# Kernel tuning notes

Hardware: AMD Instinct MI355X
Metric: run time of the kernel (lower is better)

## Reference

```python
import jax, jax.numpy as jnp
import numpy as np

N, M, D, E = 16384, 8192, 8, 2_000_000
DELTA = 1.0   # init arg delta
P = 1.0       # init arg p (forced to 1 in __init__)
EPS = 1e-6


def setup_inputs() -> dict:
    key = jax.random.key(0)
    ks = jax.random.split(key, 7)
    return {
        "gamma_rows": jax.random.normal(ks[0], (N,), dtype=jnp.float32),
        "gamma_cols": jax.random.normal(ks[1], (M,), dtype=jnp.float32),
        "latent_z": jax.random.uniform(ks[2], (N, D), dtype=jnp.float32),
        "latent_w": jax.random.uniform(ks[3], (M, D), dtype=jnp.float32),
        "weights": jax.random.uniform(ks[4], (E,), dtype=jnp.float32),
        "rows_idx": jax.random.randint(ks[5], (E,), 0, N, dtype=jnp.int32),
        "col_idx": jax.random.randint(ks[6], (E,), 0, M, dtype=jnp.int32),
    }


def reference(gamma_rows, gamma_cols, latent_z, latent_w, weights, rows_idx, col_idx):
    # Simplex projections (Softmax over latent dim)
    z = jax.nn.softmax(latent_z, axis=1)   # [N, D]
    w = jax.nn.softmax(latent_w, axis=1)   # [M, D]

    # torch.cdist(z, w, p=2): full N x M euclidean distance matrix
    sq = (jnp.sum(z * z, axis=1)[:, None]
          + jnp.sum(w * w, axis=1)[None, :]
          - 2.0 * (z @ w.T))                       # [N, M]
    dist = jnp.sqrt(jnp.maximum(sq, 0.0))          # [N, M]
    dist_matrix = -DELTA * (dist + EPS)            # [N, M]

    # z_pdist1 = exp(gamma_rows) @ exp(dist_matrix) @ exp(gamma_cols)
    z_pdist1 = jnp.einsum("i,ij,j->", jnp.exp(gamma_rows),
                          jnp.exp(dist_matrix), jnp.exp(gamma_cols))

    # Edge (link) term: per-edge euclidean distance between gathered embeddings
    delta_latent = jnp.sqrt(jnp.sum((z[rows_idx] - w[col_idx]) ** 2, axis=-1))  # [E]
    z_pdist2 = jnp.sum(weights * (gamma_rows[rows_idx] + gamma_cols[col_idx]
                                  - (DELTA * delta_latent) ** P))

    return -z_pdist2 + z_pdist1
```

## Files before the change

### kernel.cpp

```cpp
#include <hip/hip_runtime.h>
#include <math.h>

#define N_ROWS 16384
#define M_COLS 8192
#define TPB 256
#define IT 4
#define JT 64
#define JU 4
#define NJ (M_COLS / JT)
#define NIB (N_ROWS / (TPB * IT))
#define PAIR_BLOCKS (NIB * NJ)
#define EDGE_BLOCKS 2048
#define EU 4
#define GRID_BLOCKS (PAIR_BLOCKS + EDGE_BLOCKS)

typedef float v2f __attribute__((ext_vector_type(2)));
typedef _Float16 h8 __attribute__((ext_vector_type(8)));

#define C2 2.0813689810056077f

__global__ __launch_bounds__(TPB) void rownorm_kernel(
    const float* __restrict__ lz, const float* __restrict__ gr,
    const float* __restrict__ lw, const float* __restrict__ gc,
    float* __restrict__ z, float* __restrict__ zz, float* __restrict__ eg,
    _Float16* __restrict__ zh,
    float* __restrict__ w, float* __restrict__ ww, float* __restrict__ ec,
    _Float16* __restrict__ wh)
{
    int gi = blockIdx.x * TPB + threadIdx.x;
    const float *src, *g;
    float *dv, *dq, *de;
    _Float16* dh;
    int i;
    if (gi < N_ROWS) { src = lz; g = gr; dv = z; dq = zz; de = eg; dh = zh; i = gi; }
    else             { src = lw; g = gc; dv = w; dq = ww; de = ec; dh = wh; i = gi - N_ROWS; }

    const float4* sp = (const float4*)(src + (size_t)i * 8);
    float4 a = sp[0], b = sp[1];
    float v[8] = {a.x, a.y, a.z, a.w, b.x, b.y, b.z, b.w};
    float m = v[0];
    #pragma unroll
    for (int d = 1; d < 8; d++) m = fmaxf(m, v[d]);
    float s = 0.f;
    #pragma unroll
    for (int d = 0; d < 8; d++) { v[d] = __expf(v[d] - m); s += v[d]; }
    float inv = 1.f / s;
    float sq = 0.f;
    h8 hv;
    #pragma unroll
    for (int d = 0; d < 8; d++) {
        v[d] *= inv;
        sq = fmaf(v[d], v[d], sq);
        hv[d] = (_Float16)v[d];
    }
    float4 o0 = {v[0], v[1], v[2], v[3]};
    float4 o1 = {v[4], v[5], v[6], v[7]};
    float4* dp = (float4*)(dv + (size_t)i * 8);
    dp[0] = o0; dp[1] = o1;
    *(h8*)(dh + (size_t)i * 8) = hv;
    dq[i] = C2 * sq;
    de[i] = __expf(g[i]);
}

__global__ __launch_bounds__(TPB) void fused_kernel(
    const float* __restrict__ z, const float* __restrict__ zz,
    const float* __restrict__ eg,
    const float* __restrict__ w, const float* __restrict__ ww,
    const float* __restrict__ ec,
    const _Float16* __restrict__ zh, const _Float16* __restrict__ wh,
    const float* __restrict__ gr, const float* __restrict__ gc,
    const float* __restrict__ wt,
    const int* __restrict__ ridx, const int* __restrict__ cidx, int E,
    double* __restrict__ pair_part, double* __restrict__ edge_part)
{
    __shared__ float  sw[JT * 8];
    __shared__ float  swq[JT];
    __shared__ float  sec[JT];
    __shared__ double sred[TPB];

    const int t   = threadIdx.x;
    const int bid = blockIdx.x;
    const int rid = bid >> 1;

    if ((bid & 1) == 0) {
        const int ib = rid / NJ;
        const int jb = rid - ib * NJ;
        const int j0 = jb * JT;

        if (t < JT * 2) ((float4*)sw)[t] = ((const float4*)(w + (size_t)j0 * 8))[t];
        if (t < JT)     { swq[t] = ww[j0 + t]; sec[t] = ec[j0 + t]; }

        v2f  zi[IT][4];
        float zzi[IT], acc[IT];
        const int ibase = ib * (TPB * IT);
        #pragma unroll
        for (int k = 0; k < IT; k++) {
            int i = ibase + k * TPB + t;
            const float4* zp = (const float4*)(z + (size_t)i * 8);
            float4 a = zp[0], b = zp[1];
            zi[k][0] = (v2f){-2.f * C2 * a.x, -2.f * C2 * a.y};
            zi[k][1] = (v2f){-2.f * C2 * a.z, -2.f * C2 * a.w};
            zi[k][2] = (v2f){-2.f * C2 * b.x, -2.f * C2 * b.y};
            zi[k][3] = (v2f){-2.f * C2 * b.z, -2.f * C2 * b.w};
            zzi[k] = zz[i];
            acc[k] = 0.f;
        }
        __syncthreads();

        const float4* s4 = (const float4*)sw;
        for (int jo = 0; jo < JT; jo += JU) {
            float4 wa[JU], wb[JU];
            float  wq[JU], ev[JU];
            #pragma unroll
            for (int u = 0; u < JU; u++) {
                wa[u] = s4[(jo + u) * 2];
                wb[u] = s4[(jo + u) * 2 + 1];
                wq[u] = swq[jo + u];
                ev[u] = sec[jo + u];
            }
            float sq[JU][IT];
            #pragma unroll
            for (int u = 0; u < JU; u++) {
                v2f w01 = {wa[u].x, wa[u].y}, w23 = {wa[u].z, wa[u].w};
                v2f w45 = {wb[u].x, wb[u].y}, w67 = {wb[u].z, wb[u].w};
                #pragma unroll
                for (int k = 0; k < IT; k++) {
                    v2f p = {zzi[k], wq[u]};
                    p = __builtin_elementwise_fma(zi[k][0], w01, p);
                    p = __builtin_elementwise_fma(zi[k][1], w23, p);
                    p = __builtin_elementwise_fma(zi[k][2], w45, p);
                    p = __builtin_elementwise_fma(zi[k][3], w67, p);
                    sq[u][k] = fmaxf(p.x + p.y, 0.f);
                }
            }
            float dd[JU][IT];
            #pragma unroll
            for (int u = 0; u < JU; u++)
                #pragma unroll
                for (int k = 0; k < IT; k++)
                    asm("v_sqrt_f32 %0, %1" : "=v"(dd[u][k]) : "v"(sq[u][k]));
            float pr[JU][IT];
            #pragma unroll
            for (int u = 0; u < JU; u++)
                #pragma unroll
                for (int k = 0; k < IT; k++)
                    asm("v_exp_f32 %0, -%1" : "=v"(pr[u][k]) : "v"(dd[u][k]));
            #pragma unroll
            for (int u = 0; u < JU; u++)
                #pragma unroll
                for (int k = 0; k < IT; k++)
                    acc[k] = fmaf(ev[u], pr[u][k], acc[k]);
        }

        double tp = 0.0;
        #pragma unroll
        for (int k = 0; k < IT; k++) {
            int i = ibase + k * TPB + t;
            tp += (double)eg[i] * (double)acc[k];
        }

        sred[t] = tp;
        __syncthreads();
        for (int s = TPB / 2; s > 0; s >>= 1) {
            if (t < s) sred[t] += sred[t + s];
            __syncthreads();
        }
        if (t == 0) pair_part[rid] = sred[0];
    } else {
        const int tid = rid * TPB + t;
        const int e0 = tid * EU;
        double local = 0.0;
        if (e0 < E) {
            int4   rr  = *(const int4*)(ridx + e0);
            int4   cc  = *(const int4*)(cidx + e0);
            float4 wt4 = *(const float4*)(wt + e0);
            int   r[EU]  = {rr.x, rr.y, rr.z, rr.w};
            int   c[EU]  = {cc.x, cc.y, cc.z, cc.w};
            float wv[EU] = {wt4.x, wt4.y, wt4.z, wt4.w};
            h8 zr[EU], wr[EU];
            float grv[EU], gcv[EU];
            #pragma unroll
            for (int u = 0; u < EU; u++) {
                zr[u]  = *(const h8*)(zh + (size_t)r[u] * 8);
                wr[u]  = *(const h8*)(wh + (size_t)c[u] * 8);
                grv[u] = gr[r[u]];
                gcv[u] = gc[c[u]];
            }
            #pragma unroll
            for (int u = 0; u < EU; u++) {
                h8 dv = zr[u] - wr[u];
                float s = 0.f;
                #pragma unroll
                for (int qd = 0; qd < 8; qd++) {
                    float f = (float)dv[qd];
                    s = fmaf(f, f, s);
                }
                float dist;
                asm("v_sqrt_f32 %0, %1" : "=v"(dist) : "v"(s));
                local += (double)(wv[u] * (grv[u] + gcv[u] - dist));
            }
        }
        sred[t] = local;
        __syncthreads();
        for (int s2 = TPB / 2; s2 > 0; s2 >>= 1) {
            if (t < s2) sred[t] += sred[t + s2];
            __syncthreads();
        }
        if (t == 0) edge_part[rid] = sred[0];
    }
}

__global__ __launch_bounds__(TPB) void final_kernel(
    const double* __restrict__ pp, int np,
    const double* __restrict__ ep, int ne,
    float* __restrict__ out)
{
    __shared__ double sred[TPB];
    const int t = threadIdx.x;
    double s1 = 0.0, s2 = 0.0;
    for (int i = t; i < np; i += TPB) s1 += pp[i];
    for (int i = t; i < ne; i += TPB) s2 += ep[i];
    sred[t] = s1;
    __syncthreads();
    for (int s = TPB / 2; s > 0; s >>= 1) {
        if (t < s) sred[t] += sred[t + s];
        __syncthreads();
    }
    double pair_sum = sred[0];
    __syncthreads();
    sred[t] = s2;
    __syncthreads();
    for (int s = TPB / 2; s > 0; s >>= 1) {
        if (t < s) sred[t] += sred[t + s];
        __syncthreads();
    }
    if (t == 0) {
        double edge_sum = sred[0];
        double cf = exp(-1.0e-6);
        out[0] = (float)(cf * pair_sum - edge_sum);
    }
}

extern "C" void kernel_launch(void* const* d_in, const int* in_sizes, int n_in,
                              void* d_out, int out_size, void* d_ws, size_t ws_size,
                              hipStream_t stream)
{
    const float* gamma_rows = (const float*)d_in[0];
    const float* gamma_cols = (const float*)d_in[1];
    const float* latent_z   = (const float*)d_in[2];
    const float* latent_w   = (const float*)d_in[3];
    const float* weights    = (const float*)d_in[4];
    const int*   rows_idx   = (const int*)d_in[5];
    const int*   col_idx    = (const int*)d_in[6];
    float* out = (float*)d_out;
    const int E = in_sizes[4];

    char* base = (char*)d_ws;
    size_t off = 0;
    float* z  = (float*)(base + off); off += (size_t)N_ROWS * 8 * 4;
    float* zz = (float*)(base + off); off += (size_t)N_ROWS * 4;
    float* eg = (float*)(base + off); off += (size_t)N_ROWS * 4;
    float* w  = (float*)(base + off); off += (size_t)M_COLS * 8 * 4;
    float* ww = (float*)(base + off); off += (size_t)M_COLS * 4;
    float* ec = (float*)(base + off); off += (size_t)M_COLS * 4;
    _Float16* zh = (_Float16*)(base + off); off += (size_t)N_ROWS * 8 * 2;
    _Float16* wh = (_Float16*)(base + off); off += (size_t)M_COLS * 8 * 2;
    double* pair_part = (double*)(base + off); off += (size_t)PAIR_BLOCKS * 8;
    double* edge_part = (double*)(base + off); off += (size_t)EDGE_BLOCKS * 8;
    (void)ws_size;

    rownorm_kernel<<<(N_ROWS + M_COLS) / TPB, TPB, 0, stream>>>(
        latent_z, gamma_rows, latent_w, gamma_cols,
        z, zz, eg, zh, w, ww, ec, wh);
    fused_kernel<<<GRID_BLOCKS, TPB, 0, stream>>>(
        z, zz, eg, w, ww, ec, zh, wh, gamma_rows, gamma_cols,
        weights, rows_idx, col_idx, E, pair_part, edge_part);
    final_kernel<<<1, TPB, 0, stream>>>(pair_part, PAIR_BLOCKS,
                                        edge_part, EDGE_BLOCKS, out);
}
```

Baseline: 171.6 us.

## Split fused pair/edge kernel into separate launches with scalar FMAs and direct loads

Replaces the interleaved pair/edge single kernel with two separate kernels launched back to back. The pair kernel drops the shared-memory staging of w tiles and the barrier, reading w, ww and ec directly from global memory with uniform addresses (likely scalar loads). It also replaces packed v2f FMAs with scalar fmaf chains. This removes branch divergence between block types and the LDS sync, but gives up overlap between the compute-bound pair work and the memory-bound edge gathers, and may lose packed-FMA throughput.

```diff
diff --git a/kernel.cpp b/kernel.cpp
--- a/kernel.cpp
+++ b/kernel.cpp
@@ -12,9 +12,7 @@
 #define PAIR_BLOCKS (NIB * NJ)
 #define EDGE_BLOCKS 2048
 #define EU 4
-#define GRID_BLOCKS (PAIR_BLOCKS + EDGE_BLOCKS)
-
-typedef float v2f __attribute__((ext_vector_type(2)));
+
 typedef _Float16 h8 __attribute__((ext_vector_type(8)));
 
 #define C2 2.0813689810056077f
@@ -62,152 +60,142 @@
     de[i] = __expf(g[i]);
 }
 
-__global__ __launch_bounds__(TPB) void fused_kernel(
+__global__ __launch_bounds__(TPB) void pair_kernel(
     const float* __restrict__ z, const float* __restrict__ zz,
     const float* __restrict__ eg,
     const float* __restrict__ w, const float* __restrict__ ww,
     const float* __restrict__ ec,
+    double* __restrict__ pair_part)
+{
+    __shared__ double sred[TPB];
+    const int t   = threadIdx.x;
+    const int rid = blockIdx.x;
+    const int ib  = rid / NJ;
+    const int jb  = rid - ib * NJ;
+    const int j0  = jb * JT;
+
+    float zi[IT][8], zzi[IT], acc[IT];
+    const int ibase = ib * (TPB * IT);
+    #pragma unroll
+    for (int k = 0; k < IT; k++) {
+        int i = ibase + k * TPB + t;
+        const float4* zp = (const float4*)(z + (size_t)i * 8);
+        float4 a = zp[0], b = zp[1];
+        zi[k][0] = -2.f * C2 * a.x; zi[k][1] = -2.f * C2 * a.y;
+        zi[k][2] = -2.f * C2 * a.z; zi[k][3] = -2.f * C2 * a.w;
+        zi[k][4] = -2.f * C2 * b.x; zi[k][5] = -2.f * C2 * b.y;
+        zi[k][6] = -2.f * C2 * b.z; zi[k][7] = -2.f * C2 * b.w;
+        zzi[k] = zz[i];
+        acc[k] = 0.f;
+    }
+
+    const float* wb  = w  + (size_t)j0 * 8;
+    const float* wqb = ww + j0;
+    const float* ecb = ec + j0;
+
+    for (int jo = 0; jo < JT; jo += JU) {
+        float wv[JU][8], wq[JU], ev[JU];
+        #pragma unroll
+        for (int u = 0; u < JU; u++) {
+            #pragma unroll
+            for (int d = 0; d < 8; d++) wv[u][d] = wb[(jo + u) * 8 + d];
+            wq[u] = wqb[jo + u];
+            ev[u] = ecb[jo + u];
+        }
+        float sq[JU][IT];
+        #pragma unroll
+        for (int u = 0; u < JU; u++) {
+            #pragma unroll
+            for (int k = 0; k < IT; k++) {
+                float p = zzi[k] + wq[u];
+                #pragma unroll
+                for (int d = 0; d < 8; d++) p = fmaf(zi[k][d], wv[u][d], p);
+                sq[u][k] = fmaxf(p, 0.f);
+            }
+        }
+        float dd[JU][IT];
+        #pragma unroll
+        for (int u = 0; u < JU; u++)
+            #pragma unroll
+            for (int k = 0; k < IT; k++)
+                asm("v_sqrt_f32 %0, %1" : "=v"(dd[u][k]) : "v"(sq[u][k]));
+        float pr[JU][IT];
+        #pragma unroll
+        for (int u = 0; u < JU; u++)
+            #pragma unroll
+            for (int k = 0; k < IT; k++)
+                asm("v_exp_f32 %0, -%1" : "=v"(pr[u][k]) : "v"(dd[u][k]));
+        #pragma unroll
+        for (int u = 0; u < JU; u++)
+            #pragma unroll
+            for (int k = 0; k < IT; k++)
+                acc[k] = fmaf(ev[u], pr[u][k], acc[k]);
+    }
+
+    double tp = 0.0;
+    #pragma unroll
+    for (int k = 0; k < IT; k++) {
+        int i = ibase + k * TPB + t;
+        tp += (double)eg[i] * (double)acc[k];
+    }
+    sred[t] = tp;
+    __syncthreads();
+    for (int s = TPB / 2; s > 0; s >>= 1) {
+        if (t < s) sred[t] += sred[t + s];
+        __syncthreads();
+    }
+    if (t == 0) pair_part[rid] = sred[0];
+}
+
+__global__ __launch_bounds__(TPB) void edge_kernel(
     const _Float16* __restrict__ zh, const _Float16* __restrict__ wh,
     const float* __restrict__ gr, const float* __restrict__ gc,
     const float* __restrict__ wt,
     const int* __restrict__ ridx, const int* __restrict__ cidx, int E,
-    double* __restrict__ pair_part, double* __restrict__ edge_part)
-{
-    __shared__ float  sw[JT * 8];
-    __shared__ float  swq[JT];
-    __shared__ float  sec[JT];
+    double* __restrict__ edge_part)
+{
     __shared__ double sred[TPB];
-
     const int t   = threadIdx.x;
-    const int bid = blockIdx.x;
-    const int rid = bid >> 1;
-
-    if ((bid & 1) == 0) {
-        const int ib = rid / NJ;
-        const int jb = rid - ib * NJ;
-        const int j0 = jb * JT;
-
-        if (t < JT * 2) ((float4*)sw)[t] = ((const float4*)(w + (size_t)j0 * 8))[t];
-        if (t < JT)     { swq[t] = ww[j0 + t]; sec[t] = ec[j0 + t]; }
-
-        v2f  zi[IT][4];
-        float zzi[IT], acc[IT];
-        const int ibase = ib * (TPB * IT);
-        #pragma unroll
-        for (int k = 0; k < IT; k++) {
-            int i = ibase + k * TPB + t;
-            const float4* zp = (const float4*)(z + (size_t)i * 8);
-            float4 a = zp[0], b = zp[1];
-            zi[k][0] = (v2f){-2.f * C2 * a.x, -2.f * C2 * a.y};
-            zi[k][1] = (v2f){-2.f * C2 * a.z, -2.f * C2 * a.w};
-            zi[k][2] = (v2f){-2.f * C2 * b.x, -2.f * C2 * b.y};
-            zi[k][3] = (v2f){-2.f * C2 * b.z, -2.f * C2 * b.w};
-            zzi[k] = zz[i];
-            acc[k] = 0.f;
-        }
-        __syncthreads();
-
-        const float4* s4 = (const float4*)sw;
-        for (int jo = 0; jo < JT; jo += JU) {
-            float4 wa[JU], wb[JU];
-            float  wq[JU], ev[JU];
-            #pragma unroll
-            for (int u = 0; u < JU; u++) {
-                wa[u] = s4[(jo + u) * 2];
-                wb[u] = s4[(jo + u) * 2 + 1];
-                wq[u] = swq[jo + u];
-                ev[u] = sec[jo + u];
+    const int tid = blockIdx.x * TPB + t;
+    const int e0  = tid * EU;
+    double local = 0.0;
+    if (e0 < E) {
+        int4   rr  = *(const int4*)(ridx + e0);
+        int4   cc  = *(const int4*)(cidx + e0);
+        float4 wt4 = *(const float4*)(wt + e0);
+        int   r[EU]  = {rr.x, rr.y, rr.z, rr.w};
+        int   c[EU]  = {cc.x, cc.y, cc.z, cc.w};
+        float wv[EU] = {wt4.x, wt4.y, wt4.z, wt4.w};
+        h8 zr[EU], wr[EU];
+        float grv[EU], gcv[EU];
+        #pragma unroll
+        for (int u = 0; u < EU; u++) {
+            zr[u]  = *(const h8*)(zh + (size_t)r[u] * 8);
+            wr[u]  = *(const h8*)(wh + (size_t)c[u] * 8);
+            grv[u] = gr[r[u]];
+            gcv[u] = gc[c[u]];
+        }
+        #pragma unroll
+        for (int u = 0; u < EU; u++) {
+            h8 dv = zr[u] - wr[u];
+            float s = 0.f;
+            #pragma unroll
+            for (int qd = 0; qd < 8; qd++) {
+                float f = (float)dv[qd];
+                s = fmaf(f, f, s);
             }
-            float sq[JU][IT];
-            #pragma unroll
-            for (int u = 0; u < JU; u++) {
-                v2f w01 = {wa[u].x, wa[u].y}, w23 = {wa[u].z, wa[u].w};
-                v2f w45 = {wb[u].x, wb[u].y}, w67 = {wb[u].z, wb[u].w};
-                #pragma unroll
-                for (int k = 0; k < IT; k++) {
-                    v2f p = {zzi[k], wq[u]};
-                    p = __builtin_elementwise_fma(zi[k][0], w01, p);
-                    p = __builtin_elementwise_fma(zi[k][1], w23, p);
-                    p = __builtin_elementwise_fma(zi[k][2], w45, p);
-                    p = __builtin_elementwise_fma(zi[k][3], w67, p);
-                    sq[u][k] = fmaxf(p.x + p.y, 0.f);
-                }
-            }
-            float dd[JU][IT];
-            #pragma unroll
-            for (int u = 0; u < JU; u++)
-                #pragma unroll
-                for (int k = 0; k < IT; k++)
-                    asm("v_sqrt_f32 %0, %1" : "=v"(dd[u][k]) : "v"(sq[u][k]));
-            float pr[JU][IT];
-            #pragma unroll
-            for (int u = 0; u < JU; u++)
-                #pragma unroll
-                for (int k = 0; k < IT; k++)
-                    asm("v_exp_f32 %0, -%1" : "=v"(pr[u][k]) : "v"(dd[u][k]));
-            #pragma unroll
-            for (int u = 0; u < JU; u++)
-                #pragma unroll
-                for (int k = 0; k < IT; k++)
-                    acc[k] = fmaf(ev[u], pr[u][k], acc[k]);
-        }
-
-        double tp = 0.0;
-        #pragma unroll
-        for (int k = 0; k < IT; k++) {
-            int i = ibase + k * TPB + t;
-            tp += (double)eg[i] * (double)acc[k];
-        }
-
-        sred[t] = tp;
-        __syncthreads();
-        for (int s = TPB / 2; s > 0; s >>= 1) {
-            if (t < s) sred[t] += sred[t + s];
-            __syncthreads();
-        }
-        if (t == 0) pair_part[rid] = sred[0];
-    } else {
-        const int tid = rid * TPB + t;
-        const int e0 = tid * EU;
-        double local = 0.0;
-        if (e0 < E) {
-            int4   rr  = *(const int4*)(ridx + e0);
-            int4   cc  = *(const int4*)(cidx + e0);
-            float4 wt4 = *(const float4*)(wt + e0);
-            int   r[EU]  = {rr.x, rr.y, rr.z, rr.w};
-            int   c[EU]  = {cc.x, cc.y, cc.z, cc.w};
-            float wv[EU] = {wt4.x, wt4.y, wt4.z, wt4.w};
-            h8 zr[EU], wr[EU];
-            float grv[EU], gcv[EU];
-            #pragma unroll
-            for (int u = 0; u < EU; u++) {
-                zr[u]  = *(const h8*)(zh + (size_t)r[u] * 8);
-                wr[u]  = *(const h8*)(wh + (size_t)c[u] * 8);
-                grv[u] = gr[r[u]];
-                gcv[u] = gc[c[u]];
-            }
-            #pragma unroll
-            for (int u = 0; u < EU; u++) {
-                h8 dv = zr[u] - wr[u];
-                float s = 0.f;
-                #pragma unroll
-                for (int qd = 0; qd < 8; qd++) {
-                    float f = (float)dv[qd];
-                    s = fmaf(f, f, s);
-                }
-                float dist;
-                asm("v_sqrt_f32 %0, %1" : "=v"(dist) : "v"(s));
-                local += (double)(wv[u] * (grv[u] + gcv[u] - dist));
-            }
-        }
-        sred[t] = local;
-        __syncthreads();
-        for (int s2 = TPB / 2; s2 > 0; s2 >>= 1) {
-            if (t < s2) sred[t] += sred[t + s2];
-            __syncthreads();
-        }
-        if (t == 0) edge_part[rid] = sred[0];
-    }
+            float dist;
+            asm("v_sqrt_f32 %0, %1" : "=v"(dist) : "v"(s));
+            local += (double)(wv[u] * (grv[u] + gcv[u] - dist));
+        }
+    }
+    sred[t] = local;
+    __syncthreads();
+    for (int s2 = TPB / 2; s2 > 0; s2 >>= 1) {
+        if (t < s2) sred[t] += sred[t + s2];
+        __syncthreads();
+    }
+    if (t == 0) edge_part[blockIdx.x] = sred[0];
 }
 
 __global__ __launch_bounds__(TPB) void final_kernel(
@@ -272,9 +260,10 @@
     rownorm_kernel<<<(N_ROWS + M_COLS) / TPB, TPB, 0, stream>>>(
         latent_z, gamma_rows, latent_w, gamma_cols,
         z, zz, eg, zh, w, ww, ec, wh);
-    fused_kernel<<<GRID_BLOCKS, TPB, 0, stream>>>(
-        z, zz, eg, w, ww, ec, zh, wh, gamma_rows, gamma_cols,
-        weights, rows_idx, col_idx, E, pair_part, edge_part);
+    pair_kernel<<<PAIR_BLOCKS, TPB, 0, stream>>>(
+        z, zz, eg, w, ww, ec, pair_part);
+    edge_kernel<<<EDGE_BLOCKS, TPB, 0, stream>>>(
+        zh, wh, gamma_rows, gamma_cols, weights, rows_idx, col_idx, E, edge_part);
     final_kernel<<<1, TPB, 0, stream>>>(pair_part, PAIR_BLOCKS,
                                         edge_part, EDGE_BLOCKS, out);
 }
```

Result: no change. 173.4 us (+1.1%).

## Pack fp16 embedding with gamma per row, double edge unroll, rebalance block interleave

Applied to the files above, without the earlier changes.

Each row's fp16 softmax vector and its gamma value now sit together in one 32-byte record, so each edge gathers one cache line per endpoint instead of two separate random loads. The edge path handles 8 edges per thread across 1024 blocks, and blocks are interleaved two pair blocks to one edge block. The pair inner loop also moves the norm-sum add out of the FMA chain. This cuts scattered gather traffic and gives each thread more loads in flight, at the cost of more registers in edge blocks and a slightly longer dependent add in the pair loop.

```diff
diff --git a/kernel.cpp b/kernel.cpp
--- a/kernel.cpp
+++ b/kernel.cpp
@@ -10,30 +10,31 @@
 #define NJ (M_COLS / JT)
 #define NIB (N_ROWS / (TPB * IT))
 #define PAIR_BLOCKS (NIB * NJ)
-#define EDGE_BLOCKS 2048
-#define EU 4
+#define EDGE_BLOCKS 1024
+#define EU 8
 #define GRID_BLOCKS (PAIR_BLOCKS + EDGE_BLOCKS)
 
 typedef float v2f __attribute__((ext_vector_type(2)));
 typedef _Float16 h8 __attribute__((ext_vector_type(8)));
 
 #define C2 2.0813689810056077f
+#define ROWB 32
 
 __global__ __launch_bounds__(TPB) void rownorm_kernel(
     const float* __restrict__ lz, const float* __restrict__ gr,
     const float* __restrict__ lw, const float* __restrict__ gc,
     float* __restrict__ z, float* __restrict__ zz, float* __restrict__ eg,
-    _Float16* __restrict__ zh,
+    char* __restrict__ zpack,
     float* __restrict__ w, float* __restrict__ ww, float* __restrict__ ec,
-    _Float16* __restrict__ wh)
+    char* __restrict__ wpack)
 {
     int gi = blockIdx.x * TPB + threadIdx.x;
     const float *src, *g;
     float *dv, *dq, *de;
-    _Float16* dh;
+    char* dp8;
     int i;
-    if (gi < N_ROWS) { src = lz; g = gr; dv = z; dq = zz; de = eg; dh = zh; i = gi; }
-    else             { src = lw; g = gc; dv = w; dq = ww; de = ec; dh = wh; i = gi - N_ROWS; }
+    if (gi < N_ROWS) { src = lz; g = gr; dv = z; dq = zz; de = eg; dp8 = zpack; i = gi; }
+    else             { src = lw; g = gc; dv = w; dq = ww; de = ec; dp8 = wpack; i = gi - N_ROWS; }
 
     const float4* sp = (const float4*)(src + (size_t)i * 8);
     float4 a = sp[0], b = sp[1];
@@ -53,13 +54,16 @@
         sq = fmaf(v[d], v[d], sq);
         hv[d] = (_Float16)v[d];
     }
+    float gam = g[i];
     float4 o0 = {v[0], v[1], v[2], v[3]};
     float4 o1 = {v[4], v[5], v[6], v[7]};
     float4* dp = (float4*)(dv + (size_t)i * 8);
     dp[0] = o0; dp[1] = o1;
-    *(h8*)(dh + (size_t)i * 8) = hv;
     dq[i] = C2 * sq;
-    de[i] = __expf(g[i]);
+    de[i] = __expf(gam);
+    char* rp = dp8 + (size_t)i * ROWB;
+    *(h8*)rp = hv;
+    *(float*)(rp + 16) = gam;
 }
 
 __global__ __launch_bounds__(TPB) void fused_kernel(
@@ -67,8 +71,7 @@
     const float* __restrict__ eg,
     const float* __restrict__ w, const float* __restrict__ ww,
     const float* __restrict__ ec,
-    const _Float16* __restrict__ zh, const _Float16* __restrict__ wh,
-    const float* __restrict__ gr, const float* __restrict__ gc,
+    const char* __restrict__ zpack, const char* __restrict__ wpack,
     const float* __restrict__ wt,
     const int* __restrict__ ridx, const int* __restrict__ cidx, int E,
     double* __restrict__ pair_part, double* __restrict__ edge_part)
@@ -80,9 +83,11 @@
 
     const int t   = threadIdx.x;
     const int bid = blockIdx.x;
-    const int rid = bid >> 1;
-
-    if ((bid & 1) == 0) {
+    const int tri = bid / 3;
+    const int rem = bid - tri * 3;
+
+    if (rem != 0) {
+        const int rid = tri * 2 + (rem - 1);
         const int ib = rid / NJ;
         const int jb = rid - ib * NJ;
         const int j0 = jb * JT;
@@ -125,12 +130,11 @@
                 v2f w45 = {wb[u].x, wb[u].y}, w67 = {wb[u].z, wb[u].w};
                 #pragma unroll
                 for (int k = 0; k < IT; k++) {
-                    v2f p = {zzi[k], wq[u]};
-                    p = __builtin_elementwise_fma(zi[k][0], w01, p);
+                    v2f p = zi[k][0] * w01;
                     p = __builtin_elementwise_fma(zi[k][1], w23, p);
                     p = __builtin_elementwise_fma(zi[k][2], w45, p);
                     p = __builtin_elementwise_fma(zi[k][3], w67, p);
-                    sq[u][k] = fmaxf(p.x + p.y, 0.f);
+                    sq[u][k] = fmaxf(p.x + p.y + (zzi[k] + wq[u]), 0.f);
                 }
             }
             float dd[JU][IT];
@@ -158,7 +162,6 @@
             int i = ibase + k * TPB + t;
             tp += (double)eg[i] * (double)acc[k];
         }
-
         sred[t] = tp;
         __syncthreads();
         for (int s = TPB / 2; s > 0; s >>= 1) {
@@ -167,24 +170,30 @@
         }
         if (t == 0) pair_part[rid] = sred[0];
     } else {
-        const int tid = rid * TPB + t;
-        const int e0 = tid * EU;
+        const int er  = tri;
+        const int tid = er * TPB + t;
+        const int e0  = tid * EU;
         double local = 0.0;
         if (e0 < E) {
-            int4   rr  = *(const int4*)(ridx + e0);
-            int4   cc  = *(const int4*)(cidx + e0);
-            float4 wt4 = *(const float4*)(wt + e0);
-            int   r[EU]  = {rr.x, rr.y, rr.z, rr.w};
-            int   c[EU]  = {cc.x, cc.y, cc.z, cc.w};
-            float wv[EU] = {wt4.x, wt4.y, wt4.z, wt4.w};
+            int4   rr0 = *(const int4*)(ridx + e0);
+            int4   rr1 = *(const int4*)(ridx + e0 + 4);
+            int4   cc0 = *(const int4*)(cidx + e0);
+            int4   cc1 = *(const int4*)(cidx + e0 + 4);
+            float4 wtA = *(const float4*)(wt + e0);
+            float4 wtB = *(const float4*)(wt + e0 + 4);
+            int   r[EU]  = {rr0.x, rr0.y, rr0.z, rr0.w, rr1.x, rr1.y, rr1.z, rr1.w};
+            int   c[EU]  = {cc0.x, cc0.y, cc0.z, cc0.w, cc1.x, cc1.y, cc1.z, cc1.w};
+            float wv[EU] = {wtA.x, wtA.y, wtA.z, wtA.w, wtB.x, wtB.y, wtB.z, wtB.w};
             h8 zr[EU], wr[EU];
             float grv[EU], gcv[EU];
             #pragma unroll
             for (int u = 0; u < EU; u++) {
-                zr[u]  = *(const h8*)(zh + (size_t)r[u] * 8);
-                wr[u]  = *(const h8*)(wh + (size_t)c[u] * 8);
-                grv[u] = gr[r[u]];
-                gcv[u] = gc[c[u]];
+                const char* zp = zpack + (size_t)r[u] * ROWB;
+                const char* wp = wpack + (size_t)c[u] * ROWB;
+                zr[u]  = *(const h8*)zp;
+                wr[u]  = *(const h8*)wp;
+                grv[u] = *(const float*)(zp + 16);
+                gcv[u] = *(const float*)(wp + 16);
             }
             #pragma unroll
             for (int u = 0; u < EU; u++) {
@@ -206,7 +215,7 @@
             if (t < s2) sred[t] += sred[t + s2];
             __syncthreads();
         }
-        if (t == 0) edge_part[rid] = sred[0];
+        if (t == 0) edge_part[er] = sred[0];
     }
 }
 
@@ -263,17 +272,17 @@
     float* w  = (float*)(base + off); off += (size_t)M_COLS * 8 * 4;
     float* ww = (float*)(base + off); off += (size_t)M_COLS * 4;
     float* ec = (float*)(base + off); off += (size_t)M_COLS * 4;
-    _Float16* zh = (_Float16*)(base + off); off += (size_t)N_ROWS * 8 * 2;
-    _Float16* wh = (_Float16*)(base + off); off += (size_t)M_COLS * 8 * 2;
+    char* zpack = base + off; off += (size_t)N_ROWS * ROWB;
+    char* wpack = base + off; off += (size_t)M_COLS * ROWB;
     double* pair_part = (double*)(base + off); off += (size_t)PAIR_BLOCKS * 8;
     double* edge_part = (double*)(base + off); off += (size_t)EDGE_BLOCKS * 8;
     (void)ws_size;
 
     rownorm_kernel<<<(N_ROWS + M_COLS) / TPB, TPB, 0, stream>>>(
         latent_z, gamma_rows, latent_w, gamma_cols,
-        z, zz, eg, zh, w, ww, ec, wh);
+        z, zz, eg, zpack, w, ww, ec, wpack);
     fused_kernel<<<GRID_BLOCKS, TPB, 0, stream>>>(
-        z, zz, eg, w, ww, ec, zh, wh, gamma_rows, gamma_cols,
+        z, zz, eg, w, ww, ec, zpack, wpack,
         weights, rows_idx, col_idx, E, pair_part, edge_part);
     final_kernel<<<1, TPB, 0, stream>>>(pair_part, PAIR_BLOCKS,
                                         edge_part, EDGE_BLOCKS, out);
```

Measured after the change: 152.6 us. 11.0% less time.
